# Optimization experiments

Hardware: AMD Instinct MI355X
Metric: run time of the kernel (lower is better)

Reference implementation:

```python
import jax, jax.numpy as jnp
import numpy as np

N_NODES = 100000
N_EDGES = 1000000
HIDDEN = 128
N_GRAPHS = 256
EPS = 1e-6
LN_EPS = 1e-5


def _normalize(x, eps=1e-12):
    n = jnp.linalg.norm(x, axis=-1, keepdims=True)
    return x / jnp.maximum(n, eps)


def _shiftl(b, k):
    # boolean shift-left by k (positions idx-k in the torch code)
    return jnp.concatenate([b[k:], jnp.zeros((k,), dtype=bool)])


def _quaternions(R):
    Rxx, Ryy, Rzz = R[:, 0, 0], R[:, 1, 1], R[:, 2, 2]
    mag = 0.5 * jnp.sqrt(jnp.abs(1.0 + jnp.stack([Rxx - Ryy - Rzz, -Rxx + Ryy - Rzz, -Rxx - Ryy + Rzz], -1)))
    signs = jnp.sign(jnp.stack([R[:, 2, 1] - R[:, 1, 2], R[:, 0, 2] - R[:, 2, 0], R[:, 1, 0] - R[:, 0, 1]], -1))
    w = jnp.sqrt(jax.nn.relu(1.0 + Rxx + Ryy + Rzz))[:, None] / 2.0
    return _normalize(jnp.concatenate([signs * mag, w], -1))


def _layer_norm(x, g, b):
    m = jnp.mean(x, -1, keepdims=True)
    v = jnp.mean((x - m) ** 2, -1, keepdims=True)
    return (x - m) / jnp.sqrt(v + LN_EPS) * g + b


def _forward(X, batch, edge_index, W_node, b_node, g_node, beta_node, W_edge, b_edge, g_edge, beta_edge):
    N = X.shape[0]
    # bnd[i] True iff node i starts a new graph (torch: idx positions that get NaN-masked)
    bnd = jnp.concatenate([jnp.zeros((1,), dtype=bool), batch[1:] != batch[:-1]])

    # ---- dihedrals over consecutive central atoms ----
    U = _normalize(X[1:] - X[:-1])                               # [N-1,3]
    c1 = _normalize(jnp.cross(U[:-2], U[1:-1]))
    c2 = _normalize(jnp.cross(U[1:-1], U[2:]))
    cosd = jnp.clip(jnp.sum(c1 * c2, -1), -1.0 + EPS, 1.0 - EPS)
    dih = jnp.arccos(cosd) * jnp.sign(jnp.sum(c2 * U[:-2], -1))  # [N-3]
    dih = jnp.pad(dih, (1, 2))                                   # [N]; pads are masked below
    bad_d = (bnd | _shiftl(bnd, 1) | _shiftl(bnd, 2)).at[jnp.array([0, N - 2, N - 1])].set(True)
    dihedral = jnp.where(bad_d[:, None], 0.0, jnp.stack([jnp.sin(dih), jnp.cos(dih)], -1))  # [N,2]

    # ---- bond angles ----
    d0 = _normalize(X[:-2] - X[1:-1])
    d1 = _normalize(X[2:] - X[1:-1])
    cosa = jnp.sum(d0 * d1, -1)
    sina = jnp.sqrt(1.0 - cosa ** 2 + EPS)
    bad_a = (bnd | _shiftl(bnd, 1)).at[jnp.array([0, N - 1])].set(True)
    angle = jnp.where(bad_a[:, None], 0.0,
                      jnp.stack([jnp.pad(sina, (1, 1)), jnp.pad(cosa, (1, 1))], -1))        # [N,2]

    # ---- local frames Q (same invalid set as angles: idx, idx-1, 0, N-1) ----
    bvec = _normalize(U[:-1] - U[1:])
    nvec = _normalize(jnp.cross(U[:-1], U[1:]))
    Q = jnp.stack([bvec, nvec, jnp.cross(bvec, nvec)], -1)       # [N-2,3,3]
    Q = jnp.pad(Q, ((1, 1), (0, 0), (0, 0)))                     # [N,3,3]
    Q = jnp.where(bad_a[:, None, None], 0.0, Q)
    valid = ~bad_a

    # ---- edge features (gather-heavy) ----
    src, tgt = edge_index[0], edge_index[1]
    src_Q, tgt_Q = Q[src], Q[tgt]                                # [E,3,3]
    R = jnp.einsum('eji,ejk->eik', tgt_Q, src_Q)                 # tgt_Q^T @ src_Q
    orient = jnp.where((valid[src] & valid[tgt])[:, None], _quaternions(R), 0.0)            # [E,4]

    dvec = X[src] - X[tgt]
    dist = jnp.sqrt(jnp.sum(dvec ** 2, -1) + EPS)
    mu = jnp.linspace(0.0, 20.0, 16)                             # D_min=0, D_max=20, num_rbf=16
    rbf = jnp.exp(-(((dist[:, None] - mu) * (16.0 / 20.0)) ** 2))                            # [E,16]

    direct = jnp.einsum('eji,ej->ei', tgt_Q, _normalize(dvec))
    direct = jnp.where(valid[tgt][:, None], direct, 0.0)                                     # [E,3]

    h_V = jnp.concatenate([dihedral, angle], -1)                 # [N,4]
    h_E = jnp.concatenate([orient, rbf, direct], -1)             # [E,23]
    h_V = _layer_norm(h_V @ W_node + b_node, g_node, beta_node)
    h_E = _layer_norm(h_E @ W_edge + b_edge, g_edge, beta_edge)
    return h_V, h_E


def setup_inputs() -> dict:
    key = jax.random.key(0)
    ks = jax.random.split(key, 8)
    central_coords = jax.random.normal(ks[0], (N_NODES, 3), jnp.float32) * 3.0
    batch = jnp.sort(jax.random.randint(ks[1], (N_NODES,), 0, N_GRAPHS))
    edge_index = jax.random.randint(ks[2], (2, N_EDGES), 0, N_NODES)
    W_node = jax.random.normal(ks[3], (4, HIDDEN), jnp.float32) * 0.5
    b_node = jax.random.normal(ks[4], (HIDDEN,), jnp.float32) * 0.02
    W_edge = jax.random.normal(ks[5], (23, HIDDEN), jnp.float32) * 0.2
    b_edge = jax.random.normal(ks[6], (HIDDEN,), jnp.float32) * 0.02
    return dict(central_coords=central_coords, batch=batch, edge_index=edge_index,
                W_node=W_node, b_node=b_node,
                g_node=jnp.ones((HIDDEN,), jnp.float32), beta_node=jnp.zeros((HIDDEN,), jnp.float32),
                W_edge=W_edge, b_edge=b_edge,
                g_edge=jnp.ones((HIDDEN,), jnp.float32), beta_edge=jnp.zeros((HIDDEN,), jnp.float32))


def reference(central_coords, batch, edge_index, W_node, b_node, g_node, beta_node, W_edge, b_edge, g_edge, beta_edge):
    return _forward(central_coords, batch, edge_index, W_node, b_node, g_node, beta_node, W_edge, b_edge, g_edge, beta_edge)
```

## Files before the change

### kernel.cpp

```cpp
#include <hip/hip_runtime.h>
#include <math.h>

typedef __attribute__((ext_vector_type(2))) float f32x2;
typedef __attribute__((ext_vector_type(4))) float f32x4;

struct V3 { float x, y, z; };
__device__ __forceinline__ V3 v3(float a, float b, float c){ V3 r; r.x=a; r.y=b; r.z=c; return r; }
__device__ __forceinline__ V3 vsub(V3 a, V3 b){ return v3(a.x-b.x, a.y-b.y, a.z-b.z); }
__device__ __forceinline__ float vdot(V3 a, V3 b){ return a.x*b.x + a.y*b.y + a.z*b.z; }
__device__ __forceinline__ V3 vcross(V3 a, V3 b){
  return v3(a.y*b.z - a.z*b.y, a.z*b.x - a.x*b.z, a.x*b.y - a.y*b.x);
}
__device__ __forceinline__ V3 vunit(V3 a){
  float n = sqrtf(vdot(a,a));
  float inv = 1.0f / fmaxf(n, 1e-12f);
  return v3(a.x*inv, a.y*inv, a.z*inv);
}
__device__ __forceinline__ float sgnf(float x){ return (x > 0.f) ? 1.f : ((x < 0.f) ? -1.f : 0.f); }

__global__ void setup_gram(const float* __restrict__ Wn, const float* __restrict__ bn,
                           const float* __restrict__ We, const float* __restrict__ be,
                           float* __restrict__ Ge, float* __restrict__ abarE,
                           float* __restrict__ Gn, float* __restrict__ abarN)
{
  int tid = threadIdx.x;
  if (tid < 576) {
    int i = tid / 24, j = tid % 24;
    const float* ai = (i < 23) ? (We + i * 128) : be;
    const float* aj = (j < 23) ? (We + j * 128) : be;
    float s = 0.f;
    for (int c = 0; c < 128; ++c) s += ai[c] * aj[c];
    Ge[tid] = s * (1.0f / 128.0f);
  } else if (tid < 601) {
    int t = tid - 576; int i = t / 5, j = t % 5;
    const float* ai = (i < 4) ? (Wn + i * 128) : bn;
    const float* aj = (j < 4) ? (Wn + j * 128) : bn;
    float s = 0.f;
    for (int c = 0; c < 128; ++c) s += ai[c] * aj[c];
    Gn[t] = s * (1.0f / 128.0f);
  } else if (tid < 625) {
    int k = tid - 601;
    const float* a = (k < 23) ? (We + k * 128) : be;
    float s = 0.f;
    for (int c = 0; c < 128; ++c) s += a[c];
    abarE[k] = s * (1.0f / 128.0f);
  } else if (tid < 630) {
    int k = tid - 625;
    const float* a = (k < 4) ? (Wn + k * 128) : bn;
    float s = 0.f;
    for (int c = 0; c < 128; ++c) s += a[c];
    abarN[k] = s * (1.0f / 128.0f);
  }
}

__global__ __launch_bounds__(256, 4) void node_kernel(
    const float* __restrict__ X, const int* __restrict__ batch,
    const float* __restrict__ Wn, const float* __restrict__ bn,
    const float* __restrict__ gn, const float* __restrict__ betan,
    const float* __restrict__ Gn, const float* __restrict__ abarN,
    float* __restrict__ Qws, int* __restrict__ validws,
    float* __restrict__ outV, int N)
{
  __shared__ float smem[256 * 8];

  int lane = threadIdx.x & 63;
  int wave = threadIdx.x >> 6;
  int base = blockIdx.x * 256 + wave * 64;
  int i = base + lane;
  bool live = (i < N);
  int ic = live ? i : (N - 1);

  int im1 = (ic >= 1) ? ic - 1 : 0;
  int ip1 = (ic + 1 < N) ? ic + 1 : N - 1;
  int ip2 = (ic + 2 < N) ? ic + 2 : N - 1;

  V3 xm1 = v3(X[3*im1], X[3*im1+1], X[3*im1+2]);
  V3 x0  = v3(X[3*ic ], X[3*ic +1], X[3*ic +2]);
  V3 xp1 = v3(X[3*ip1], X[3*ip1+1], X[3*ip1+2]);
  V3 xp2 = v3(X[3*ip2], X[3*ip2+1], X[3*ip2+2]);

  int b0 = batch[ic];
  bool bnd_i  = (ic >= 1)    && (batch[ic - 1] != b0);
  bool bnd_i1 = (ic + 1 < N) && (batch[ic + 1] != b0);
  bool bnd_i2 = (ic + 2 < N) && (batch[ic + 2] != batch[ic + 1]);

  bool bad_d = bnd_i || bnd_i1 || bnd_i2 || (ic == 0) || (ic >= N - 2);
  bool bad_a = bnd_i || bnd_i1 || (ic == 0) || (ic == N - 1);

  V3 u0 = vunit(vsub(x0,  xm1));
  V3 u1 = vunit(vsub(xp1, x0 ));
  V3 u2 = vunit(vsub(xp2, xp1));
  V3 c1 = vunit(vcross(u0, u1));
  V3 c2 = vunit(vcross(u1, u2));

  float cosd = vdot(c1, c2);
  cosd = fminf(fmaxf(cosd, -1.0f + 1e-6f), 1.0f - 1e-6f);
  float sd = vdot(c2, u0);
  float f0, f1;
  if (bad_d)          { f0 = 0.f; f1 = 0.f; }
  else {
    float sg = sgnf(sd);
    if (sg == 0.f)    { f0 = 0.f; f1 = 1.f; }
    else              { f0 = sg * sqrtf(fmaxf(1.f - cosd * cosd, 0.f)); f1 = cosd; }
  }

  V3 d0 = vunit(vsub(xm1, x0));
  V3 d1 = vunit(vsub(xp1, x0));
  float cosa = vdot(d0, d1);
  float sina = sqrtf(fmaxf(1.0f - cosa * cosa + 1e-6f, 0.f));
  float f2 = bad_a ? 0.f : sina;
  float f3 = bad_a ? 0.f : cosa;

  V3 bv = vunit(vsub(u0, u1));
  V3 nv = c1;
  V3 tv = vcross(bv, nv);
  float q[9];
  if (bad_a) {
    #pragma unroll
    for (int k = 0; k < 9; ++k) q[k] = 0.f;
  } else {
    q[0]=bv.x; q[1]=nv.x; q[2]=tv.x;
    q[3]=bv.y; q[4]=nv.y; q[5]=tv.y;
    q[6]=bv.z; q[7]=nv.z; q[8]=tv.z;
  }
  if (live) {
    f32x4* qp = (f32x4*)(Qws + (size_t)i * 12);
    f32x4 ca; ca.x=q[0]; ca.y=q[1]; ca.z=q[2]; ca.w=q[3];
    f32x4 cb; cb.x=q[4]; cb.y=q[5]; cb.z=q[6]; cb.w=q[7];
    f32x4 cc; cc.x=q[8]; cc.y=x0.x; cc.z=x0.y; cc.w=x0.z;
    qp[0] = ca; qp[1] = cb; qp[2] = cc;
    validws[i] = bad_a ? 0 : 1;
  }

  float fa[5] = { f0, f1, f2, f3, 1.0f };
  float mmean = 0.f;
  #pragma unroll
  for (int k = 0; k < 5; ++k) mmean = fmaf(fa[k], abarN[k], mmean);
  float E2 = 0.f;
  #pragma unroll
  for (int ii = 0; ii < 5; ++ii) {
    float ti = 0.f;
    #pragma unroll
    for (int jj = 0; jj < 5; ++jj) ti = fmaf(Gn[ii * 5 + jj], fa[jj], ti);
    E2 = fmaf(fa[ii], ti, E2);
  }
  float var  = fmaxf(E2 - mmean * mmean, 0.f);
  float rstd = rsqrtf(var + 1e-5f);

  {
    f32x4* rowp = (f32x4*)(smem + (int)threadIdx.x * 8);
    f32x4 v0; v0.x = f0; v0.y = f1; v0.z = f2; v0.w = f3;
    f32x4 v1; v1.x = mmean; v1.y = rstd; v1.z = 0.f; v1.w = 0.f;
    rowp[0] = v0; rowp[1] = v1;
  }

  f32x2 W2[4];
  #pragma unroll
  for (int k = 0; k < 4; ++k) W2[k] = *(const f32x2*)(Wn + k * 128 + 2 * lane);
  f32x2 b2 = *(const f32x2*)(bn    + 2 * lane);
  f32x2 g2 = *(const f32x2*)(gn    + 2 * lane);
  f32x2 e2 = *(const f32x2*)(betan + 2 * lane);

  __syncthreads();

  int nIt = N - base; nIt = (nIt > 64) ? 64 : nIt;
  const float* rp = smem + (wave * 64) * 8;
  float* op = outV + (size_t)base * 128 + 2 * lane;
  #pragma unroll 2
  for (int t = 0; t < nIt; ++t) {
    f32x4 v0 = *(const f32x4*)(rp + 0);
    f32x4 v1 = *(const f32x4*)(rp + 4);
    float bm = v1.x, br = v1.y;
    f32x2 acc = b2;
    f32x2 s0 = v0.x, s1 = v0.y, s2 = v0.z, s3 = v0.w;
    acc = __builtin_elementwise_fma(s0, W2[0], acc);
    acc = __builtin_elementwise_fma(s1, W2[1], acc);
    acc = __builtin_elementwise_fma(s2, W2[2], acc);
    acc = __builtin_elementwise_fma(s3, W2[3], acc);
    f32x2 out;
    out.x = (acc.x - bm) * br * g2.x + e2.x;
    out.y = (acc.y - bm) * br * g2.y + e2.y;
    *(f32x2*)op = out;
    rp += 8; op += 128;
  }
}

__global__ __launch_bounds__(256, 4) void edge_kernel(
    const int* __restrict__ eidx,
    const float* __restrict__ We, const float* __restrict__ be,
    const float* __restrict__ ge, const float* __restrict__ betae,
    const float* __restrict__ Qws, const int* __restrict__ validws,
    const float* __restrict__ Ge, const float* __restrict__ abarE,
    float* __restrict__ outE, int N, int E)
{
  __shared__ float smem[256 * 36];

  int lane = threadIdx.x & 63;
  int wave = threadIdx.x >> 6;
  int base = blockIdx.x * 256 + wave * 64;
  int e = base + lane;
  int ec = (e < E) ? e : (E - 1);

  int s = eidx[ec];
  int t = eidx[E + ec];

  const f32x4* sp = (const f32x4*)(Qws + (size_t)s * 12);
  const f32x4* tp = (const f32x4*)(Qws + (size_t)t * 12);
  f32x4 sA = sp[0], sB = sp[1], sC = sp[2];
  f32x4 tA = tp[0], tB = tp[1], tC = tp[2];

  float Qs[9] = { sA.x, sA.y, sA.z, sA.w, sB.x, sB.y, sB.z, sB.w, sC.x };
  float Qt[9] = { tA.x, tA.y, tA.z, tA.w, tB.x, tB.y, tB.z, tB.w, tC.x };
  float Xs0 = sC.y, Xs1 = sC.z, Xs2 = sC.w;
  float Xt0 = tC.y, Xt1 = tC.z, Xt2 = tC.w;
  int ok = validws[s] & validws[t];

  float R[9];
  #pragma unroll
  for (int i = 0; i < 3; ++i) {
    #pragma unroll
    for (int k = 0; k < 3; ++k) {
      R[3*i+k] = Qt[i] * Qs[k] + Qt[3+i] * Qs[3+k] + Qt[6+i] * Qs[6+k];
    }
  }

  float Rxx = R[0], Ryy = R[4], Rzz = R[8];
  float m0 = 0.5f * sqrtf(fabsf(1.f + Rxx - Ryy - Rzz));
  float m1 = 0.5f * sqrtf(fabsf(1.f - Rxx + Ryy - Rzz));
  float m2 = 0.5f * sqrtf(fabsf(1.f - Rxx - Ryy + Rzz));
  float s0 = sgnf(R[7] - R[5]);
  float s1 = sgnf(R[2] - R[6]);
  float s2 = sgnf(R[3] - R[1]);
  float w  = 0.5f * sqrtf(fmaxf(1.f + Rxx + Ryy + Rzz, 0.f));
  float q0 = s0 * m0, q1 = s1 * m1, q2 = s2 * m2;
  float qn = fmaxf(sqrtf(q0*q0 + q1*q1 + q2*q2 + w*w), 1e-12f);
  float qinv = 1.0f / qn;
  float msk = ok ? 1.f : 0.f;

  float f[23];
  f[0] = q0 * qinv * msk; f[1] = q1 * qinv * msk;
  f[2] = q2 * qinv * msk; f[3] = w  * qinv * msk;

  float dx = Xs0 - Xt0, dy = Xs1 - Xt1, dz = Xs2 - Xt2;
  float d2 = dx*dx + dy*dy + dz*dz;
  float dist = sqrtf(d2 + 1e-6f);
  #pragma unroll
  for (int k = 0; k < 16; ++k) {
    float u = (dist - (float)k * (20.0f / 15.0f)) * 0.8f;
    f[4 + k] = __expf(-u * u);
  }
  float dn = fmaxf(sqrtf(d2), 1e-12f);
  float rinv = 1.0f / dn;
  float ux = dx * rinv, uy = dy * rinv, uz = dz * rinv;
  f[20] = Qt[0]*ux + Qt[3]*uy + Qt[6]*uz;
  f[21] = Qt[1]*ux + Qt[4]*uy + Qt[7]*uz;
  f[22] = Qt[2]*ux + Qt[5]*uy + Qt[8]*uz;

  float mmean = abarE[23];
  #pragma unroll
  for (int k = 0; k < 23; ++k) mmean = fmaf(f[k], abarE[k], mmean);
  float E2 = 0.f;
  #pragma unroll
  for (int ii = 0; ii < 24; ++ii) {
    float fi = (ii < 23) ? f[ii] : 1.0f;
    float ti = 0.f;
    #pragma unroll
    for (int jj = 0; jj < 24; ++jj) {
      float fj = (jj < 23) ? f[jj] : 1.0f;
      ti = fmaf(Ge[ii * 24 + jj], fj, ti);
    }
    E2 = fmaf(fi, ti, E2);
  }
  float var  = fmaxf(E2 - mmean * mmean, 0.f);
  float rstd = rsqrtf(var + 1e-5f);

  {
    f32x4* rowp = (f32x4*)(smem + (int)threadIdx.x * 36);
    f32x4 v;
    v.x = f[0];  v.y = f[1];  v.z = f[2];  v.w = f[3];  rowp[0] = v;
    v.x = f[4];  v.y = f[5];  v.z = f[6];  v.w = f[7];  rowp[1] = v;
    v.x = f[8];  v.y = f[9];  v.z = f[10]; v.w = f[11]; rowp[2] = v;
    v.x = f[12]; v.y = f[13]; v.z = f[14]; v.w = f[15]; rowp[3] = v;
    v.x = f[16]; v.y = f[17]; v.z = f[18]; v.w = f[19]; rowp[4] = v;
    v.x = f[20]; v.y = f[21]; v.z = f[22]; v.w = mmean; rowp[5] = v;
    v.x = rstd;  v.y = 0.f;   v.z = 0.f;   v.w = 0.f;   rowp[6] = v;
  }

  f32x2 Wc[23];
  #pragma unroll
  for (int k = 0; k < 23; ++k) Wc[k] = *(const f32x2*)(We + k * 128 + 2 * lane);
  f32x2 b2 = *(const f32x2*)(be    + 2 * lane);
  f32x2 g2 = *(const f32x2*)(ge    + 2 * lane);
  f32x2 e2 = *(const f32x2*)(betae + 2 * lane);

  __syncthreads();

  int nIt = E - base; nIt = (nIt > 64) ? 64 : nIt;
  const float* rp = smem + (wave * 64) * 36;
  float* op = outE + (size_t)base * 128 + 2 * lane;
  #pragma unroll 2
  for (int tt = 0; tt < nIt; ++tt) {
    f32x4 c0 = *(const f32x4*)(rp + 0);
    f32x4 c1 = *(const f32x4*)(rp + 4);
    f32x4 c2 = *(const f32x4*)(rp + 8);
    f32x4 c3 = *(const f32x4*)(rp + 12);
    f32x4 c4 = *(const f32x4*)(rp + 16);
    f32x4 c5 = *(const f32x4*)(rp + 20);
    f32x4 c6 = *(const f32x4*)(rp + 24);
    float fs[23] = { c0.x, c0.y, c0.z, c0.w,
                     c1.x, c1.y, c1.z, c1.w,
                     c2.x, c2.y, c2.z, c2.w,
                     c3.x, c3.y, c3.z, c3.w,
                     c4.x, c4.y, c4.z, c4.w,
                     c5.x, c5.y, c5.z };
    float bm = c5.w, br = c6.x;
    f32x2 acc = b2;
    #pragma unroll
    for (int k = 0; k < 23; ++k) {
      f32x2 sv = fs[k];
      acc = __builtin_elementwise_fma(sv, Wc[k], acc);
    }
    f32x2 out;
    out.x = (acc.x - bm) * br * g2.x + e2.x;
    out.y = (acc.y - bm) * br * g2.y + e2.y;
    *(f32x2*)op = out;
    rp += 36; op += 128;
  }
}

extern "C" void kernel_launch(void* const* d_in, const int* in_sizes, int n_in,
                              void* d_out, int out_size, void* d_ws, size_t ws_size,
                              hipStream_t stream)
{
  const float* X     = (const float*)d_in[0];
  const int*   batch = (const int*)  d_in[1];
  const int*   eidx  = (const int*)  d_in[2];
  const float* Wn    = (const float*)d_in[3];
  const float* bn    = (const float*)d_in[4];
  const float* gn    = (const float*)d_in[5];
  const float* betan = (const float*)d_in[6];
  const float* We    = (const float*)d_in[7];
  const float* be    = (const float*)d_in[8];
  const float* ge    = (const float*)d_in[9];
  const float* betae = (const float*)d_in[10];

  int N = in_sizes[0] / 3;
  int E = in_sizes[2] / 2;

  float* ws      = (float*)d_ws;
  float* Qws     = ws;
  int*   validws = (int*)(ws + (size_t)N * 12);
  float* Ge      = ws + (size_t)N * 12 + N;
  float* abarE   = Ge + 576;
  float* Gn      = abarE + 24;
  float* abarN   = Gn + 25;

  float* outV = (float*)d_out;
  float* outE = outV + (size_t)N * 128;

  hipLaunchKernelGGL(setup_gram, dim3(1), dim3(640), 0, stream,
                     Wn, bn, We, be, Ge, abarE, Gn, abarN);

  int nblocks = (N + 255) / 256;
  hipLaunchKernelGGL(node_kernel, dim3(nblocks), dim3(256), 0, stream,
                     X, batch, Wn, bn, gn, betan, Gn, abarN, Qws, validws, outV, N);

  int eblocks = (E + 255) / 256;
  hipLaunchKernelGGL(edge_kernel, dim3(eblocks), dim3(256), 0, stream,
                     eidx, We, be, ge, betae, Qws, validws, Ge, abarE, outE, N, E);
}
```

Baseline: 631.6 us.

## Compute edge outputs as 4 columns per lane over two rows per wave

```diff
diff --git a/kernel.cpp b/kernel.cpp
--- a/kernel.cpp
+++ b/kernel.cpp
@@ -185,7 +185,7 @@
   }
 }
 
-__global__ __launch_bounds__(256, 4) void edge_kernel(
+__global__ __launch_bounds__(256, 3) void edge_kernel(
     const int* __restrict__ eidx,
     const float* __restrict__ We, const float* __restrict__ be,
     const float* __restrict__ ge, const float* __restrict__ betae,
@@ -193,7 +193,7 @@
     const float* __restrict__ Ge, const float* __restrict__ abarE,
     float* __restrict__ outE, int N, int E)
 {
-  __shared__ float smem[256 * 36];
+  __shared__ float smem[256 * 28];
 
   int lane = threadIdx.x & 63;
   int wave = threadIdx.x >> 6;
@@ -275,7 +275,8 @@
   float rstd = rsqrtf(var + 1e-5f);
 
   {
-    f32x4* rowp = (f32x4*)(smem + (int)threadIdx.x * 36);
+    float* rowf = smem + (int)threadIdx.x * 28;
+    f32x4* rowp = (f32x4*)rowf;
     f32x4 v;
     v.x = f[0];  v.y = f[1];  v.z = f[2];  v.w = f[3];  rowp[0] = v;
     v.x = f[4];  v.y = f[5];  v.z = f[6];  v.w = f[7];  rowp[1] = v;
@@ -283,48 +284,53 @@
     v.x = f[12]; v.y = f[13]; v.z = f[14]; v.w = f[15]; rowp[3] = v;
     v.x = f[16]; v.y = f[17]; v.z = f[18]; v.w = f[19]; rowp[4] = v;
     v.x = f[20]; v.y = f[21]; v.z = f[22]; v.w = mmean; rowp[5] = v;
-    v.x = rstd;  v.y = 0.f;   v.z = 0.f;   v.w = 0.f;   rowp[6] = v;
-  }
-
-  f32x2 Wc[23];
-  #pragma unroll
-  for (int k = 0; k < 23; ++k) Wc[k] = *(const f32x2*)(We + k * 128 + 2 * lane);
-  f32x2 b2 = *(const f32x2*)(be    + 2 * lane);
-  f32x2 g2 = *(const f32x2*)(ge    + 2 * lane);
-  f32x2 e2 = *(const f32x2*)(betae + 2 * lane);
+    rowf[24] = rstd;
+  }
+
+  int half = lane >> 5;
+  int cq   = (lane & 31) * 4;
+  f32x4 Wc[23];
+  #pragma unroll
+  for (int k = 0; k < 23; ++k) Wc[k] = *(const f32x4*)(We + k * 128 + cq);
+  f32x4 b4 = *(const f32x4*)(be    + cq);
+  f32x4 g4 = *(const f32x4*)(ge    + cq);
+  f32x4 e4 = *(const f32x4*)(betae + cq);
 
   __syncthreads();
 
   int nIt = E - base; nIt = (nIt > 64) ? 64 : nIt;
-  const float* rp = smem + (wave * 64) * 36;
-  float* op = outE + (size_t)base * 128 + 2 * lane;
-  #pragma unroll 2
-  for (int tt = 0; tt < nIt; ++tt) {
+  const float* rp = smem + (wave * 64 + half) * 28;
+  float* op = outE + (size_t)(base + half) * 128 + cq;
+  for (int tt = 0; tt < 32; ++tt) {
+    int rel = 2 * tt + half;
+    if (rel >= nIt) break;
     f32x4 c0 = *(const f32x4*)(rp + 0);
     f32x4 c1 = *(const f32x4*)(rp + 4);
     f32x4 c2 = *(const f32x4*)(rp + 8);
     f32x4 c3 = *(const f32x4*)(rp + 12);
     f32x4 c4 = *(const f32x4*)(rp + 16);
     f32x4 c5 = *(const f32x4*)(rp + 20);
-    f32x4 c6 = *(const f32x4*)(rp + 24);
+    float br = rp[24];
+    float bm = c5.w;
     float fs[23] = { c0.x, c0.y, c0.z, c0.w,
                      c1.x, c1.y, c1.z, c1.w,
                      c2.x, c2.y, c2.z, c2.w,
                      c3.x, c3.y, c3.z, c3.w,
                      c4.x, c4.y, c4.z, c4.w,
                      c5.x, c5.y, c5.z };
-    float bm = c5.w, br = c6.x;
-    f32x2 acc = b2;
+    f32x4 acc = b4;
     #pragma unroll
     for (int k = 0; k < 23; ++k) {
-      f32x2 sv = fs[k];
+      f32x4 sv = fs[k];
       acc = __builtin_elementwise_fma(sv, Wc[k], acc);
     }
-    f32x2 out;
-    out.x = (acc.x - bm) * br * g2.x + e2.x;
-    out.y = (acc.y - bm) * br * g2.y + e2.y;
-    *(f32x2*)op = out;
-    rp += 36; op += 128;
+    f32x4 out;
+    out.x = (acc.x - bm) * br * g4.x + e4.x;
+    out.y = (acc.y - bm) * br * g4.y + e4.y;
+    out.z = (acc.z - bm) * br * g4.z + e4.z;
+    out.w = (acc.w - bm) * br * g4.w + e4.w;
+    *(f32x4*)op = out;
+    rp += 2 * 28; op += 2 * 128;
   }
 }
 
```

New measurement: 625.9 us. No clear change (-0.9%).
